# Kernel optimization log

Measured on AMD Instinct MI355X. Metric: run time of the kernel, lower is better.

Reference implementation:

```python
import jax, jax.numpy as jnp
import numpy as np

HEADS = 16
KEY_SIZE = 64
SIZE_PER_HEAD = 64
D_MODEL = 1024
OUT_DIM = HEADS * SIZE_PER_HEAD
NEG_BIG = 1e10


def setup_inputs() -> dict:
    key = jax.random.key(0)
    ks = jax.random.split(key, 8)
    B, S = 4, 2048
    q = jax.random.normal(ks[0], (B, S, D_MODEL), dtype=jnp.float32)
    k = jax.random.normal(ks[1], (B, S, D_MODEL), dtype=jnp.float32)
    v = jax.random.normal(ks[2], (B, S, D_MODEL), dtype=jnp.float32)
    # binary masks (1 = keep), as floats like the Keras layer expects
    v_mask = (jax.random.uniform(ks[3], (B, S)) > 0.1).astype(jnp.float32)
    q_mask = (jax.random.uniform(ks[4], (B, S)) > 0.1).astype(jnp.float32)
    sc = 1.0 / np.sqrt(D_MODEL)
    Wq = jax.random.normal(ks[5], (D_MODEL, HEADS * KEY_SIZE), dtype=jnp.float32) * sc
    Wk = jax.random.normal(ks[6], (D_MODEL, HEADS * KEY_SIZE), dtype=jnp.float32) * sc
    Wv = jax.random.normal(ks[7], (D_MODEL, OUT_DIM), dtype=jnp.float32) * sc
    return {"q": q, "k": k, "v": v, "v_mask": v_mask, "q_mask": q_mask,
            "Wq": Wq, "Wk": Wk, "Wv": Wv}


def reference(q, k, v, v_mask, q_mask, Wq, Wk, Wv):
    B, Sq, _ = q.shape
    Sk = k.shape[1]
    # projections -> [B, H, S, d]
    qw = (q @ Wq).reshape(B, Sq, HEADS, KEY_SIZE).transpose(0, 2, 1, 3)
    kw = (k @ Wk).reshape(B, Sk, HEADS, KEY_SIZE).transpose(0, 2, 1, 3)
    vw = (v @ Wv).reshape(B, Sk, HEADS, SIZE_PER_HEAD).transpose(0, 2, 1, 3)
    # scaled scores [B, H, Sq, Sk]
    a = jnp.einsum('bhqd,bhkd->bhqk', qw, kw) / np.sqrt(KEY_SIZE).astype(np.float32)
    # additive key-side mask (v_mask broadcasts over heads and query axis)
    a = a - (1.0 - v_mask[:, None, None, :]) * NEG_BIG
    # causal (mask_right): subtract big value on strictly upper triangle
    causal = jnp.triu(jnp.ones((Sq, Sk), dtype=a.dtype), k=1) * NEG_BIG
    a = a - causal[None, None]
    a = jax.nn.softmax(a, axis=-1)
    o = jnp.einsum('bhqk,bhkd->bhqd', a, vw)
    o = o.transpose(0, 2, 1, 3).reshape(B, Sq, OUT_DIM)
    # multiplicative query-side mask
    o = o * q_mask[:, :, None]
    return o
```

## Files before the change

kernel.cpp:

```cpp
#include <hip/hip_runtime.h>
#include <hip/hip_bf16.h>

typedef __bf16 bf16x8 __attribute__((ext_vector_type(8)));
typedef float f32x4 __attribute__((ext_vector_type(4)));
typedef unsigned int u32;
typedef u32 u32x4 __attribute__((ext_vector_type(4)));

#define MFMA16(a, b, c) __builtin_amdgcn_mfma_f32_16x16x32_bf16(a, b, c, 0, 0, 0)

static __device__ __forceinline__ unsigned short f2b(float f) {
    __hip_bfloat16 b = __float2bfloat16(f);
    return __builtin_bit_cast(unsigned short, b);
}
static __device__ __forceinline__ float b2f(unsigned short u) {
    u32 v = ((u32)u) << 16;
    return __builtin_bit_cast(float, v);
}
static __device__ __forceinline__ u32 pk2(float lo, float hi) {
    return (__builtin_bit_cast(u32, lo) >> 16) | (__builtin_bit_cast(u32, hi) & 0xFFFF0000u);
}
static __device__ __forceinline__ void glds16(const void* g, void* l) {
    __builtin_amdgcn_global_load_lds((const __attribute__((address_space(1))) u32*)g,
                                     (__attribute__((address_space(3))) u32*)l, 16, 0, 0);
}
static __device__ __forceinline__ int vperm(int t) {
    return (t & 32) | ((t & 12) << 1) | ((t & 16) >> 2) | (t & 3);
}

__global__ __launch_bounds__(256) void cvt2_kernel(const float* __restrict__ s0,
        const float* __restrict__ s1, unsigned short* __restrict__ d0,
        unsigned short* __restrict__ d1) {
    const float* src = blockIdx.y ? s1 : s0;
    unsigned short* dst = blockIdx.y ? d1 : d0;
    const size_t i = ((size_t)blockIdx.x * 256 + threadIdx.x) * 8;
    float4 a = *(const float4*)(src + i);
    float4 b = *(const float4*)(src + i + 4);
    ushort4 u0 = { f2b(a.x), f2b(a.y), f2b(a.z), f2b(a.w) };
    ushort4 u1 = { f2b(b.x), f2b(b.y), f2b(b.z), f2b(b.w) };
    *(ushort4*)(dst + i) = u0;
    *(ushort4*)(dst + i + 4) = u1;
}

__global__ void wt_kernel(const float* __restrict__ W0, const float* __restrict__ W1,
                          const float* __restrict__ W2, unsigned short* __restrict__ T0,
                          unsigned short* __restrict__ T1, unsigned short* __restrict__ T2) {
    const float* W = blockIdx.z == 0 ? W0 : (blockIdx.z == 1 ? W1 : W2);
    unsigned short* T = blockIdx.z == 0 ? T0 : (blockIdx.z == 1 ? T1 : T2);
    __shared__ float tile[32][33];
    const int n0 = blockIdx.x * 32, k0 = blockIdx.y * 32;
    const int tx = threadIdx.x, ty = threadIdx.y;
#pragma unroll
    for (int i = 0; i < 4; i++)
        tile[ty + 8 * i][tx] = W[(size_t)(k0 + ty + 8 * i) * 1024 + n0 + tx];
    __syncthreads();
#pragma unroll
    for (int i = 0; i < 4; i++)
        T[(size_t)(n0 + ty + 8 * i) * 1024 + k0 + tx] = f2b(tile[tx][ty + 8 * i]);
}

__global__ __launch_bounds__(256) void proj_kernel(
        const unsigned short* __restrict__ A0, const unsigned short* __restrict__ A1,
        const unsigned short* __restrict__ W0, const unsigned short* __restrict__ W1,
        unsigned short* __restrict__ D0, unsigned short* __restrict__ D1, const int vmode) {
    __shared__ unsigned short smem[17408];
    unsigned short* As = smem;
    unsigned short* Bs = smem + 8192;
    const unsigned short* A  = blockIdx.z ? A1 : A0;
    const unsigned short* Wt = blockIdx.z ? W1 : W0;
    unsigned short* dst      = blockIdx.z ? D1 : D0;
    const int m0 = blockIdx.x * 128, n0 = blockIdx.y * 128;
    const int tid = threadIdx.x;
    const int w = tid >> 6, lane = tid & 63, quad = lane >> 4, l16 = lane & 15;
    const int wr = (w >> 1) * 64, wc = (w & 1) * 64;
    const unsigned short* ap[4];
    const unsigned short* bp[4];
#pragma unroll
    for (int i = 0; i < 4; i++) {
        int idx = tid + i * 256;
        int row = (idx >> 2) & 127, ch = (idx >> 9) * 4 + (idx & 3);
        ap[i] = A + (size_t)(m0 + row) * 1024 + ch * 8;
        bp[i] = Wt + (size_t)(n0 + row) * 1024 + ch * 8;
    }
    f32x4 acc[4][4] = {};
    for (int kb = 0; kb < 16; kb++) {
        __syncthreads();
#pragma unroll
        for (int i = 0; i < 4; i++) {
            glds16(ap[i], &As[(tid + i * 256) * 8]);
            glds16(bp[i], &Bs[(tid + i * 256) * 8]);
            ap[i] += 64; bp[i] += 64;
        }
        __syncthreads();
#pragma unroll
        for (int kp = 0; kp < 2; kp++) {
            bf16x8 af[4], bf[4];
#pragma unroll
            for (int mt = 0; mt < 4; mt++)
                af[mt] = *(const bf16x8*)&As[kp * 4096 + (wr + mt * 16 + l16) * 32 + quad * 8];
#pragma unroll
            for (int nt = 0; nt < 4; nt++)
                bf[nt] = *(const bf16x8*)&Bs[kp * 4096 + (wc + nt * 16 + l16) * 32 + quad * 8];
#pragma unroll
            for (int mt = 0; mt < 4; mt++)
#pragma unroll
                for (int nt = 0; nt < 4; nt++)
                    acc[mt][nt] = MFMA16(af[mt], bf[nt], acc[mt][nt]);
        }
    }
    __syncthreads();
    unsigned short* Tw = smem + w * 4352;
    if (vmode == 0) {
#pragma unroll
        for (int mt = 0; mt < 4; mt++)
#pragma unroll
            for (int nt = 0; nt < 4; nt++)
#pragma unroll
                for (int r = 0; r < 4; r++)
                    Tw[(mt * 16 + quad * 4 + r) * 68 + nt * 16 + l16] = f2b(acc[mt][nt][r]);
    } else {
#pragma unroll
        for (int mt = 0; mt < 4; mt++)
#pragma unroll
            for (int nt = 0; nt < 4; nt++)
#pragma unroll
                for (int r = 0; r < 4; r++)
                    Tw[(nt * 16 + l16) * 68 + vperm(mt * 16 + quad * 4 + r)] = f2b(acc[mt][nt][r]);
    }
    const int gr0 = m0 + wr, gc0 = n0 + wc;
    const int b = gr0 >> 11, s0 = gr0 & 2047, h = gc0 >> 6;
    if (vmode == 0) {
        const size_t obase = (size_t)(b * 16 + h) * 2048;
#pragma unroll
        for (int j = 0; j < 16; j++) {
            int row = j * 4 + quad;
            uint2 val = *(const uint2*)&Tw[row * 68 + l16 * 4];
            *(uint2*)(dst + (obase + s0 + row) * 64 + l16 * 4) = val;
        }
    } else {
        const size_t vbase = (size_t)(b * 16 + h) * 64 * 2048;
#pragma unroll
        for (int j = 0; j < 16; j++) {
            int row = j * 4 + quad;
            uint2 val = *(const uint2*)&Tw[row * 68 + l16 * 4];
            *(uint2*)(dst + vbase + (size_t)row * 2048 + s0 + l16 * 4) = val;
        }
    }
}

__global__ __launch_bounds__(256) void attn_kernel(
        const unsigned short* __restrict__ Qp, const unsigned short* __restrict__ Kp,
        const unsigned short* __restrict__ Vt, const float* __restrict__ vmask,
        const float* __restrict__ qmask, float* __restrict__ out) {
    __shared__ unsigned short Ks[4096];
    __shared__ unsigned short Vts[4096];
    __shared__ float Vmb[2048];
    const int bh = blockIdx.x, b = bh >> 4, h = bh & 15;
    const int tid = threadIdx.x;
    const int w = tid >> 6, lane = tid & 63, quad = lane >> 4, l16 = lane & 15;
    const size_t base = (size_t)bh * 2048 * 64;
    const float C1 = 0.18033688f;
    const float C0 = -11.54156036f;
    const float CM = -1.44269504e10f;
    for (int i = tid; i < 2048; i += 256)
        Vmb[i] = (vmask[b * 2048 + i] != 0.f) ? C0 : (C0 + CM);

    const int i0 = tid, i1 = tid + 256;
    const unsigned short* kp0 = Kp + base + (size_t)((i0 >> 2) & 63) * 64 + (i0 >> 8) * 32 + (i0 & 3) * 8;
    const unsigned short* kp1 = Kp + base + (size_t)((i1 >> 2) & 63) * 64 + (i1 >> 8) * 32 + (i1 & 3) * 8;
    const unsigned short* vp0 = Vt + base + (size_t)((i0 >> 2) & 63) * 2048 + (i0 >> 8) * 32 + (i0 & 3) * 8;
    const unsigned short* vp1 = Vt + base + (size_t)((i1 >> 2) & 63) * 2048 + (i1 >> 8) * 32 + (i1 & 3) * 8;

    for (int pass = 0; pass < 2; pass++) {
        const int qt = pass ? 15 - blockIdx.y : blockIdx.y;
        const int q0 = qt * 128;
        bf16x8 qa[2][2];
#pragma unroll
        for (int qc = 0; qc < 2; qc++)
#pragma unroll
            for (int ks = 0; ks < 2; ks++)
                qa[qc][ks] = *(const bf16x8*)(Qp + base +
                    (size_t)(q0 + w * 32 + qc * 16 + l16) * 64 + ks * 32 + quad * 8);
        f32x4 o[2][4] = {};
        float lsum[2] = {0.f, 0.f};

        auto do_tile = [&](int kt, bool diag) __attribute__((always_inline)) {
            __syncthreads();
            glds16(kp0 + (size_t)kt * 4096, &Ks[i0 * 8]);
            glds16(kp1 + (size_t)kt * 4096, &Ks[i1 * 8]);
            glds16(vp0 + kt * 64, &Vts[i0 * 8]);
            glds16(vp1 + kt * 64, &Vts[i1 * 8]);
            __syncthreads();

            f32x4 st[2][4];
#pragma unroll
            for (int nt = 0; nt < 4; nt++) {
                bf16x8 kf0 = *(const bf16x8*)&Ks[(nt * 16 + l16) * 32 + quad * 8];
                bf16x8 kf1 = *(const bf16x8*)&Ks[2048 + (nt * 16 + l16) * 32 + quad * 8];
#pragma unroll
                for (int qc = 0; qc < 2; qc++) {
                    f32x4 z = {};
                    z = MFMA16(kf0, qa[qc][0], z);
                    z = MFMA16(kf1, qa[qc][1], z);
                    st[qc][nt] = z;
                }
            }
            float p[2][4][4];
#pragma unroll
            for (int nt = 0; nt < 4; nt++) {
                f32x4 vb4 = *(const f32x4*)&Vmb[kt * 64 + nt * 16 + quad * 4];
#pragma unroll
                for (int qc = 0; qc < 2; qc++) {
                    const int thr = w * 32 + qc * 16 + l16 - (kt - 2 * qt) * 64;
#pragma unroll
                    for (int r = 0; r < 4; r++) {
                        float pv = __builtin_amdgcn_exp2f(st[qc][nt][r] * C1 + vb4[r]);
                        if (diag)
                            pv = (nt * 16 + quad * 4 + r > thr) ? 0.f : pv;
                        p[qc][nt][r] = pv;
                        lsum[qc] += pv;
                    }
                }
            }
#pragma unroll
            for (int h2 = 0; h2 < 2; h2++) {
                bf16x8 pa[2];
#pragma unroll
                for (int qc = 0; qc < 2; qc++) {
                    u32x4 pw = { pk2(p[qc][2 * h2][0], p[qc][2 * h2][1]),
                                 pk2(p[qc][2 * h2][2], p[qc][2 * h2][3]),
                                 pk2(p[qc][2 * h2 + 1][0], p[qc][2 * h2 + 1][1]),
                                 pk2(p[qc][2 * h2 + 1][2], p[qc][2 * h2 + 1][3]) };
                    pa[qc] = __builtin_bit_cast(bf16x8, pw);
                }
#pragma unroll
                for (int dt = 0; dt < 4; dt++) {
                    bf16x8 vb = *(const bf16x8*)&Vts[h2 * 2048 + (dt * 16 + l16) * 32 + quad * 8];
#pragma unroll
                    for (int qc = 0; qc < 2; qc++)
                        o[qc][dt] = MFMA16(pa[qc], vb, o[qc][dt]);
                }
            }
        };
        for (int kt = 0; kt < 2 * qt; kt++) do_tile(kt, false);
        do_tile(2 * qt, true);
        do_tile(2 * qt + 1, true);

        float lr[2][4];
#pragma unroll
        for (int qc = 0; qc < 2; qc++) {
            float lf = lsum[qc];
            lf += __shfl_xor(lf, 16);
            lf += __shfl_xor(lf, 32);
#pragma unroll
            for (int r = 0; r < 4; r++) lr[qc][r] = __shfl(lf, quad * 4 + r);
        }
        bool deg = false;
#pragma unroll
        for (int qc = 0; qc < 2; qc++)
#pragma unroll
            for (int r = 0; r < 4; r++) deg |= (lr[qc][r] == 0.f);
        if (__any((int)deg)) {
#pragma unroll
            for (int qc = 0; qc < 2; qc++)
#pragma unroll
                for (int r = 0; r < 4; r++)
                    if (lr[qc][r] == 0.f) {
                        const int qr = q0 + w * 32 + qc * 16 + quad * 4 + r;
                        float cnt = 0.f;
                        float oacc[4] = {0.f, 0.f, 0.f, 0.f};
                        for (int kv = 0; kv < 2048; kv++) {
                            bool keep = (kv <= qr) || (vmask[b * 2048 + kv] != 0.f);
                            if (keep) {
                                int col = (kv & ~63) | vperm(kv & 63);
                                cnt += 1.f;
#pragma unroll
                                for (int dt = 0; dt < 4; dt++)
                                    oacc[dt] += b2f(Vt[base + (size_t)(dt * 16 + l16) * 2048 + col]);
                            }
                        }
                        lr[qc][r] = cnt;
#pragma unroll
                        for (int dt = 0; dt < 4; dt++) o[qc][dt][r] = oacc[dt];
                    }
        }
#pragma unroll
        for (int qc = 0; qc < 2; qc++)
#pragma unroll
            for (int r = 0; r < 4; r++) {
                int q = q0 + w * 32 + qc * 16 + quad * 4 + r;
                float sc = qmask[b * 2048 + q] / lr[qc][r];
#pragma unroll
                for (int dt = 0; dt < 4; dt++)
                    out[(size_t)(b * 2048 + q) * 1024 + h * 64 + dt * 16 + l16] = o[qc][dt][r] * sc;
            }
    }
}

extern "C" void kernel_launch(void* const* d_in, const int* in_sizes, int n_in,
                              void* d_out, int out_size, void* d_ws, size_t ws_size,
                              hipStream_t stream) {
    const float* q  = (const float*)d_in[0];
    const float* k  = (const float*)d_in[1];
    const float* v  = (const float*)d_in[2];
    const float* vm = (const float*)d_in[3];
    const float* qm = (const float*)d_in[4];
    const float* Wq = (const float*)d_in[5];
    const float* Wk = (const float*)d_in[6];
    const float* Wv = (const float*)d_in[7];
    float* out = (float*)d_out;

    unsigned short* ws  = (unsigned short*)d_ws;
    unsigned short* Wtq = ws;
    unsigned short* Wtk = Wtq + (1u << 20);
    unsigned short* Wtv = Wtk + (1u << 20);
    unsigned short* Qp  = Wtv + (1u << 20);
    unsigned short* Kp  = Qp + (1u << 23);
    unsigned short* Vtp = Kp + (1u << 23);
    unsigned short* Aq = (unsigned short*)d_out;
    unsigned short* Ak = Aq + (1u << 23);

    wt_kernel<<<dim3(32, 32, 3), dim3(32, 8), 0, stream>>>(Wq, Wk, Wv, Wtq, Wtk, Wtv);
    cvt2_kernel<<<dim3(4096, 2), 256, 0, stream>>>(q, k, Aq, Ak);
    proj_kernel<<<dim3(64, 8, 2), 256, 0, stream>>>(Aq, Ak, Wtq, Wtk, Qp, Kp, 0);
    cvt2_kernel<<<dim3(4096, 1), 256, 0, stream>>>(v, v, Aq, Aq);
    proj_kernel<<<dim3(64, 8, 1), 256, 0, stream>>>(Aq, Aq, Wtv, Wtv, Vtp, Vtp, 1);
    attn_kernel<<<dim3(64, 8), 256, 0, stream>>>(Qp, Kp, Vtp, vm, qm, out);
}
```

Baseline: 278.1 us.

## Double-buffer K/V tiles in attention and batch Q/K/V projections into one launch

The attention kernel now keeps two LDS buffers for K and V tiles and prefetches the next tile while computing the current one, so there is one barrier per tile instead of two and global-load latency can overlap with MFMA work. When the workspace is large enough, the q/k/v conversions and projections are merged into single launches over three z-slices, with v's bf16 copy placed in the workspace, removing two kernel launches and the serialization between them. This costs extra LDS in attention, which may lower occupancy, and depends on the workspace-size check to choose the path.

```diff
diff --git a/kernel.cpp b/kernel.cpp
--- a/kernel.cpp
+++ b/kernel.cpp
@@ -27,11 +27,13 @@
     return (t & 32) | ((t & 12) << 1) | ((t & 16) >> 2) | (t & 3);
 }
 
-__global__ __launch_bounds__(256) void cvt2_kernel(const float* __restrict__ s0,
-        const float* __restrict__ s1, unsigned short* __restrict__ d0,
-        unsigned short* __restrict__ d1) {
-    const float* src = blockIdx.y ? s1 : s0;
-    unsigned short* dst = blockIdx.y ? d1 : d0;
+__global__ __launch_bounds__(256) void cvt3_kernel(const float* __restrict__ s0,
+        const float* __restrict__ s1, const float* __restrict__ s2,
+        unsigned short* __restrict__ d0, unsigned short* __restrict__ d1,
+        unsigned short* __restrict__ d2) {
+    const int z = blockIdx.y;
+    const float* src = z == 0 ? s0 : (z == 1 ? s1 : s2);
+    unsigned short* dst = z == 0 ? d0 : (z == 1 ? d1 : d2);
     const size_t i = ((size_t)blockIdx.x * 256 + threadIdx.x) * 8;
     float4 a = *(const float4*)(src + i);
     float4 b = *(const float4*)(src + i + 4);
@@ -60,14 +62,19 @@
 
 __global__ __launch_bounds__(256) void proj_kernel(
         const unsigned short* __restrict__ A0, const unsigned short* __restrict__ A1,
+        const unsigned short* __restrict__ A2,
         const unsigned short* __restrict__ W0, const unsigned short* __restrict__ W1,
-        unsigned short* __restrict__ D0, unsigned short* __restrict__ D1, const int vmode) {
+        const unsigned short* __restrict__ W2,
+        unsigned short* __restrict__ D0, unsigned short* __restrict__ D1,
+        unsigned short* __restrict__ D2, const int zoff) {
     __shared__ unsigned short smem[17408];
     unsigned short* As = smem;
     unsigned short* Bs = smem + 8192;
-    const unsigned short* A  = blockIdx.z ? A1 : A0;
-    const unsigned short* Wt = blockIdx.z ? W1 : W0;
-    unsigned short* dst      = blockIdx.z ? D1 : D0;
+    const int z = blockIdx.z;
+    const unsigned short* A  = z == 0 ? A0 : (z == 1 ? A1 : A2);
+    const unsigned short* Wt = z == 0 ? W0 : (z == 1 ? W1 : W2);
+    unsigned short* dst      = z == 0 ? D0 : (z == 1 ? D1 : D2);
+    const int vmode = (z + zoff == 2);
     const int m0 = blockIdx.x * 128, n0 = blockIdx.y * 128;
     const int tid = threadIdx.x;
     const int w = tid >> 6, lane = tid & 63, quad = lane >> 4, l16 = lane & 15;
@@ -151,8 +158,8 @@
         const unsigned short* __restrict__ Qp, const unsigned short* __restrict__ Kp,
         const unsigned short* __restrict__ Vt, const float* __restrict__ vmask,
         const float* __restrict__ qmask, float* __restrict__ out) {
-    __shared__ unsigned short Ks[4096];
-    __shared__ unsigned short Vts[4096];
+    __shared__ unsigned short Ks[2][4096];
+    __shared__ unsigned short Vts[2][4096];
     __shared__ float Vmb[2048];
     const int bh = blockIdx.x, b = bh >> 4, h = bh & 15;
     const int tid = threadIdx.x;
@@ -183,19 +190,18 @@
         f32x4 o[2][4] = {};
         float lsum[2] = {0.f, 0.f};
 
-        auto do_tile = [&](int kt, bool diag) __attribute__((always_inline)) {
-            __syncthreads();
-            glds16(kp0 + (size_t)kt * 4096, &Ks[i0 * 8]);
-            glds16(kp1 + (size_t)kt * 4096, &Ks[i1 * 8]);
-            glds16(vp0 + kt * 64, &Vts[i0 * 8]);
-            glds16(vp1 + kt * 64, &Vts[i1 * 8]);
-            __syncthreads();
-
+        auto stage = [&](int kt, int sel) __attribute__((always_inline)) {
+            glds16(kp0 + (size_t)kt * 4096, &Ks[sel][i0 * 8]);
+            glds16(kp1 + (size_t)kt * 4096, &Ks[sel][i1 * 8]);
+            glds16(vp0 + kt * 64, &Vts[sel][i0 * 8]);
+            glds16(vp1 + kt * 64, &Vts[sel][i1 * 8]);
+        };
+        auto compute = [&](int kt, int sel, bool diag) __attribute__((always_inline)) {
             f32x4 st[2][4];
 #pragma unroll
             for (int nt = 0; nt < 4; nt++) {
-                bf16x8 kf0 = *(const bf16x8*)&Ks[(nt * 16 + l16) * 32 + quad * 8];
-                bf16x8 kf1 = *(const bf16x8*)&Ks[2048 + (nt * 16 + l16) * 32 + quad * 8];
+                bf16x8 kf0 = *(const bf16x8*)&Ks[sel][(nt * 16 + l16) * 32 + quad * 8];
+                bf16x8 kf1 = *(const bf16x8*)&Ks[sel][2048 + (nt * 16 + l16) * 32 + quad * 8];
 #pragma unroll
                 for (int qc = 0; qc < 2; qc++) {
                     f32x4 z = {};
@@ -234,16 +240,22 @@
                 }
 #pragma unroll
                 for (int dt = 0; dt < 4; dt++) {
-                    bf16x8 vb = *(const bf16x8*)&Vts[h2 * 2048 + (dt * 16 + l16) * 32 + quad * 8];
+                    bf16x8 vb = *(const bf16x8*)&Vts[sel][h2 * 2048 + (dt * 16 + l16) * 32 + quad * 8];
 #pragma unroll
                     for (int qc = 0; qc < 2; qc++)
                         o[qc][dt] = MFMA16(pa[qc], vb, o[qc][dt]);
                 }
             }
         };
-        for (int kt = 0; kt < 2 * qt; kt++) do_tile(kt, false);
-        do_tile(2 * qt, true);
-        do_tile(2 * qt + 1, true);
+
+        const int ntiles = 2 * qt + 2;
+        __syncthreads();
+        stage(0, 0);
+        for (int kt = 0; kt < ntiles; kt++) {
+            __syncthreads();
+            if (kt + 1 < ntiles) stage(kt + 1, (kt + 1) & 1);
+            compute(kt, kt & 1, kt >= 2 * qt);
+        }
 
         float lr[2][4];
 #pragma unroll
@@ -316,13 +328,22 @@
     unsigned short* Qp  = Wtv + (1u << 20);
     unsigned short* Kp  = Qp + (1u << 23);
     unsigned short* Vtp = Kp + (1u << 23);
+    unsigned short* Av  = Vtp + (1u << 23);
     unsigned short* Aq = (unsigned short*)d_out;
     unsigned short* Ak = Aq + (1u << 23);
 
     wt_kernel<<<dim3(32, 32, 3), dim3(32, 8), 0, stream>>>(Wq, Wk, Wv, Wtq, Wtk, Wtv);
-    cvt2_kernel<<<dim3(4096, 2), 256, 0, stream>>>(q, k, Aq, Ak);
-    proj_kernel<<<dim3(64, 8, 2), 256, 0, stream>>>(Aq, Ak, Wtq, Wtk, Qp, Kp, 0);
-    cvt2_kernel<<<dim3(4096, 1), 256, 0, stream>>>(v, v, Aq, Aq);
-    proj_kernel<<<dim3(64, 8, 1), 256, 0, stream>>>(Aq, Aq, Wtv, Wtv, Vtp, Vtp, 1);
+    if (ws_size >= 73400320u) {
+        cvt3_kernel<<<dim3(4096, 3), 256, 0, stream>>>(q, k, v, Aq, Ak, Av);
+        proj_kernel<<<dim3(64, 8, 3), 256, 0, stream>>>(Aq, Ak, Av, Wtq, Wtk, Wtv,
+                                                        Qp, Kp, Vtp, 0);
+    } else {
+        cvt3_kernel<<<dim3(4096, 2), 256, 0, stream>>>(q, k, v, Aq, Ak, Ak);
+        proj_kernel<<<dim3(64, 8, 2), 256, 0, stream>>>(Aq, Ak, Ak, Wtq, Wtk, Wtk,
+                                                        Qp, Kp, Kp, 0);
+        cvt3_kernel<<<dim3(4096, 1), 256, 0, stream>>>(v, v, v, Aq, Aq, Aq);
+        proj_kernel<<<dim3(64, 8, 1), 256, 0, stream>>>(Aq, Aq, Aq, Wtv, Wtv, Wtv,
+                                                        Vtp, Vtp, Vtp, 2);
+    }
     attn_kernel<<<dim3(64, 8), 256, 0, stream>>>(Qp, Kp, Vtp, vm, qm, out);
 }
```

New measurement: 274.0 us. Within noise of the previous version (-1.5%).
